# Performance work log

Hardware: AMD Instinct MI355X
Metric: run time of the kernel (lower is better)

## Reference

```python
import jax, jax.numpy as jnp
import numpy as np

V, E, H, L, S, B = 32000, 512, 1024, 2, 512, 32


def setup_inputs() -> dict:
    key = jax.random.key(0)
    ks = jax.random.split(key, 12)
    s = 0.05  # keep activations in a sane range
    return {
        "x": jax.random.randint(ks[0], (S, B), 0, V),
        "embed": jax.random.normal(ks[1], (V, E), dtype=jnp.float32) * s,
        "W_ih0": jax.random.normal(ks[2], (4 * H, E), dtype=jnp.float32) * s,
        "W_hh0": jax.random.normal(ks[3], (4 * H, H), dtype=jnp.float32) * s,
        "b_ih0": jax.random.normal(ks[4], (4 * H,), dtype=jnp.float32) * s,
        "b_hh0": jax.random.normal(ks[5], (4 * H,), dtype=jnp.float32) * s,
        "W_ih1": jax.random.normal(ks[6], (4 * H, H), dtype=jnp.float32) * s,
        "W_hh1": jax.random.normal(ks[7], (4 * H, H), dtype=jnp.float32) * s,
        "b_ih1": jax.random.normal(ks[8], (4 * H,), dtype=jnp.float32) * s,
        "b_hh1": jax.random.normal(ks[9], (4 * H,), dtype=jnp.float32) * s,
        "h0": jax.random.normal(ks[10], (L, B, H), dtype=jnp.float32) * s,
        "c0": jax.random.normal(ks[11], (L, B, H), dtype=jnp.float32) * s,
    }


def _lstm_cell(x_t, h_prev, c_prev, Wi, Wh, bi, bh):
    # PyTorch gate order: input, forget, cell(g), output
    gates = x_t @ Wi.T + h_prev @ Wh.T + bi + bh  # [B, 4H]
    i, f, g, o = jnp.split(gates, 4, axis=-1)
    i = jax.nn.sigmoid(i)
    f = jax.nn.sigmoid(f)
    g = jnp.tanh(g)
    o = jax.nn.sigmoid(o)
    c_new = f * c_prev + i * g
    h_new = o * jnp.tanh(c_new)
    return h_new, c_new


def reference(x, embed, W_ih0, W_hh0, b_ih0, b_hh0,
              W_ih1, W_hh1, b_ih1, b_hh1, h0, c0):
    emb = embed[x]  # [S, B, E]; dropout p=0.0 -> identity
    layers = ((W_ih0, W_hh0, b_ih0, b_hh0), (W_ih1, W_hh1, b_ih1, b_hh1))

    def step(carry, e_t):
        h, c = carry  # each [L, B, H]
        inp = e_t
        new_h, new_c = [], []
        for l, (Wi, Wh, bi, bh) in enumerate(layers):
            h_l, c_l = _lstm_cell(inp, h[l], c[l], Wi, Wh, bi, bh)
            new_h.append(h_l)
            new_c.append(c_l)
            inp = h_l  # inter-layer dropout p=0.0 -> identity
        h = jnp.stack(new_h)
        c = jnp.stack(new_c)
        return (h, c), (inp, h, c)

    (_, _), (outs, hiddens, cells) = jax.lax.scan(step, (h0, c0), emb)
    outputs = outs[:, None, :, :]  # match torch shape [S, 1, B, H]
    return outputs, hiddens, cells
```

## Files before the change

### kernel.cpp

```cpp
#include <hip/hip_runtime.h>
#include <hip/hip_cooperative_groups.h>

namespace cg = cooperative_groups;


#define S_LEN 512
#define BATCH 32
#define HID   1024
#define EMB   512
#define NBLK  128
#define NTHR  512

typedef short  bf16x8 __attribute__((ext_vector_type(8)));
typedef float  f32x4  __attribute__((ext_vector_type(4)));

union U8 { bf16x8 v; unsigned short us[8]; uint4 u4; unsigned long long ull[2]; };

__device__ __forceinline__ unsigned short f2bf(float f) {
    unsigned u = __float_as_uint(f);
    u += 0x7fffu + ((u >> 16) & 1u);
    return (unsigned short)(u >> 16);
}

__device__ __forceinline__ uint4 pack8(float4 lo, float4 hi) {
    U8 r;
    r.us[0] = f2bf(lo.x); r.us[1] = f2bf(lo.y); r.us[2] = f2bf(lo.z); r.us[3] = f2bf(lo.w);
    r.us[4] = f2bf(hi.x); r.us[5] = f2bf(hi.y); r.us[6] = f2bf(hi.z); r.us[7] = f2bf(hi.w);
    return r.u4;
}

__device__ __forceinline__ f32x4 mfma16(bf16x8 a, bf16x8 b, f32x4 c) {
    return __builtin_amdgcn_mfma_f32_16x16x32_bf16(a, b, c, 0, 0, 0);
}

__device__ __forceinline__ U8 ld_ws16(const uint4* p) {
    const unsigned long long* q = (const unsigned long long*)p;
    U8 r;
    r.ull[0] = __hip_atomic_load(q,     __ATOMIC_RELAXED, __HIP_MEMORY_SCOPE_AGENT);
    r.ull[1] = __hip_atomic_load(q + 1, __ATOMIC_RELAXED, __HIP_MEMORY_SCOPE_AGENT);
    return r;
}
__device__ __forceinline__ void st_ws16(uint4* p, U8 v) {
    unsigned long long* q = (unsigned long long*)p;
    __hip_atomic_store(q,     v.ull[0], __ATOMIC_RELAXED, __HIP_MEMORY_SCOPE_AGENT);
    __hip_atomic_store(q + 1, v.ull[1], __ATOMIC_RELAXED, __HIP_MEMORY_SCOPE_AGENT);
}

__device__ __forceinline__ float sigm(float x) {
    return __builtin_amdgcn_rcpf(1.0f + __expf(-x));
}
__device__ __forceinline__ float tanh_fast(float x) {
    const float xc = fminf(fmaxf(x, -15.f), 15.f);
    const float t  = __expf(2.f * xc);
    return (t - 1.f) * __builtin_amdgcn_rcpf(t + 1.f);
}

__device__ __forceinline__ void poll64(const int* flags, int target) {
    const int* p = flags + ((threadIdx.x & 63) << 4);
    for (;;) {
        const int v = __hip_atomic_load(p, __ATOMIC_RELAXED, __HIP_MEMORY_SCOPE_AGENT);
        if (__all(v >= target)) break;
        __builtin_amdgcn_s_sleep(1);
    }
}

__global__ __launch_bounds__(NTHR, 1)
void lstm_pipe(const int* __restrict__ x, const float* __restrict__ embed,
               const float* __restrict__ Wi0, const float* __restrict__ Wh0,
               const float* __restrict__ bi0, const float* __restrict__ bh0,
               const float* __restrict__ Wi1, const float* __restrict__ Wh1,
               const float* __restrict__ bi1, const float* __restrict__ bh1,
               const float* __restrict__ h0in, const float* __restrict__ c0in,
               float* __restrict__ outputs, float* __restrict__ hiddens,
               float* __restrict__ cells, uint4* __restrict__ ws)
{
    __shared__ f32x4 sRed[8][8][64];
    __shared__ float sGates[32][68];
    __shared__ unsigned short sHex[32][16];
    __shared__ float sBias[16][4];
    uint4* sEmb = (uint4*)&sRed[0][0][0];

    const int tid  = threadIdx.x;
    const int lane = tid & 63;
    const int wv   = tid >> 6;
    const int bx   = blockIdx.x;
    const bool isL0 = (bx < 64);
    const int g    = isL0 ? bx : bx - 64;

    uint4* h0base = ws;
    uint4* h1base = ws + 16384;
    int*   fbase  = (int*)(ws + 24576);
    int*   flag0  = fbase;
    int*   flag1  = fbase + 1024;

    {
        const int gt = bx * NTHR + tid;
        if (gt < 2048) fbase[gt] = 0;
        if (gt < 8192) {
            const int layer = gt >> 12, kg = (gt >> 5) & 127, b = gt & 31;
            const float* src = h0in + (((size_t)layer << 5) + b) * HID + (kg << 3);
            uint4* dst = layer ? (h1base + 4096) : (h0base + 3 * 4096);
            dst[(kg << 5) + b] = pack8(*(const float4*)src, *(const float4*)(src + 4));
        }
    }
    if (tid < 16) {
        #pragma unroll
        for (int gate = 0; gate < 4; ++gate) {
            const int r = (gate << 10) + (g << 4) + tid;
            sBias[tid][gate] = isL0 ? (bi0[r] + bh0[r]) : (bi1[r] + bh1[r]);
        }
    }
    const int pjj = tid & 15;
    const int pb  = tid >> 4;
    const int jg  = (g << 4) + pjj;
    float creg = isL0 ? c0in[(size_t)pb * HID + jg]
                      : c0in[(size_t)(BATCH + pb) * HID + jg];

    const int n_    = lane & 15;
    const int ko_   = (lane >> 4) << 3;
    const int rb_   = ((n_ >> 2) << 10) + (g << 4) + (n_ & 3);
    bf16x8 w0[4][6];
    bf16x8 w1[4][8];
    if (isL0) {
        #pragma unroll
        for (int nt = 0; nt < 4; ++nt) {
            const int r = rb_ + (nt << 2);
            #pragma unroll
            for (int kf = 0; kf < 6; ++kf) {
                const int k = wv * 192 + kf * 32 + ko_;
                const float* src = (k < EMB) ? Wi0 + (size_t)r * EMB + k
                                             : Wh0 + (size_t)r * HID + (k - EMB);
                U8 t; t.u4 = pack8(*(const float4*)src, *(const float4*)(src + 4));
                w0[nt][kf] = t.v;
            }
        }
    } else {
        #pragma unroll
        for (int nt = 0; nt < 4; ++nt) {
            const int r = rb_ + (nt << 2);
            #pragma unroll
            for (int kf = 0; kf < 8; ++kf) {
                const int k = (wv << 8) + kf * 32 + ko_;
                const float* src = (k < HID) ? Wi1 + (size_t)r * HID + k
                                             : Wh1 + (size_t)r * HID + (k - HID);
                U8 t; t.u4 = pack8(*(const float4*)src, *(const float4*)(src + 4));
                w1[nt][kf] = t.v;
            }
        }
    }

    float4 pe[4][2];
    if (isL0) {
        #pragma unroll
        for (int it = 0; it < 4; ++it) {
            const int b = wv + (it << 3);
            const float* src = embed + (size_t)x[b] * EMB + (lane << 3);
            pe[it][0] = *(const float4*)src;
            pe[it][1] = *(const float4*)(src + 4);
        }
    }

    cg::grid_group grid = cg::this_grid();
    grid.sync();

    const size_t BH = (size_t)BATCH * HID;

    if (isL0) {
        for (int s = 0; s < S_LEN; ++s) {
            #pragma unroll
            for (int it = 0; it < 4; ++it)
                sEmb[lane * 33 + wv + (it << 3)] = pack8(pe[it][0], pe[it][1]);
            __syncthreads();

            if (s + 1 < S_LEN) {
                #pragma unroll
                for (int it = 0; it < 4; ++it) {
                    const int b = wv + (it << 3);
                    const float* src = embed + (size_t)x[((s + 1) << 5) + b] * EMB + (lane << 3);
                    pe[it][0] = *(const float4*)src;
                    pe[it][1] = *(const float4*)(src + 4);
                }
            }
            if (wv >= 2) poll64(flag0, s);

            const uint4* h0p = h0base + (((s + 3) & 3) << 12);

            U8 r0[6], r1[6];
            #pragma unroll
            for (int kf = 0; kf < 6; ++kf) {
                const int kfg = wv * 6 + kf;
                if (kfg >= 16) {
                    const int u = (((kfg - 16) << 2) + (lane >> 4)) * 32 + (lane & 15);
                    r0[kf] = ld_ws16(&h0p[u]);
                    r1[kf] = ld_ws16(&h0p[u + 16]);
                }
            }
            f32x4 acc[2][4] = {{{0,0,0,0},{0,0,0,0},{0,0,0,0},{0,0,0,0}},
                               {{0,0,0,0},{0,0,0,0},{0,0,0,0},{0,0,0,0}}};
            #pragma unroll
            for (int kf = 0; kf < 6; ++kf) {
                const int kfg = wv * 6 + kf;
                bf16x8 a0, a1;
                if (kfg < 16) {
                    const int u = ((kfg << 2) + (lane >> 4)) * 33 + (lane & 15);
                    U8 t0; t0.u4 = sEmb[u];      a0 = t0.v;
                    U8 t1; t1.u4 = sEmb[u + 16]; a1 = t1.v;
                } else {
                    a0 = r0[kf].v;
                    a1 = r1[kf].v;
                }
                #pragma unroll
                for (int nt = 0; nt < 4; ++nt) {
                    acc[0][nt] = mfma16(a0, w0[nt][kf], acc[0][nt]);
                    acc[1][nt] = mfma16(a1, w0[nt][kf], acc[1][nt]);
                }
            }
            __syncthreads();
            #pragma unroll
            for (int mt = 0; mt < 2; ++mt)
                #pragma unroll
                for (int nt = 0; nt < 4; ++nt)
                    sRed[wv][(mt << 2) + nt][lane] = acc[mt][nt];
            __syncthreads();
            {
                const int tile = tid >> 6, l = tid & 63;
                f32x4 sum = sRed[0][tile][l];
                #pragma unroll
                for (int w = 1; w < 8; ++w) sum += sRed[w][tile][l];
                const int mt = tile >> 2, nt = tile & 3;
                const int b0 = (mt << 4) + ((l >> 4) << 2);
                const int col = (nt << 4) + (l & 15);
                sGates[b0 + 0][col] = sum[0];
                sGates[b0 + 1][col] = sum[1];
                sGates[b0 + 2][col] = sum[2];
                sGates[b0 + 3][col] = sum[3];
            }
            __syncthreads();
            float cn_out, hn_out;
            {
                const int cb = ((pjj >> 2) << 4) + (pjj & 3);
                const float ii = sigm     (sGates[pb][cb]      + sBias[pjj][0]);
                const float ff = sigm     (sGates[pb][cb + 4]  + sBias[pjj][1]);
                const float gg = tanh_fast(sGates[pb][cb + 8]  + sBias[pjj][2]);
                const float oo = sigm     (sGates[pb][cb + 12] + sBias[pjj][3]);
                cn_out = ff * creg + ii * gg;
                creg = cn_out;
                hn_out = oo * tanh_fast(cn_out);
                sHex[pb][pjj] = f2bf(hn_out);
            }
            __syncthreads();
            if (wv == 0) {
                if (s >= 4) poll64(flag1, s - 3);
                const int b = lane & 31, kgl = lane >> 5;
                U8 hb;
                #pragma unroll
                for (int jj = 0; jj < 8; ++jj) hb.us[jj] = sHex[b][(kgl << 3) + jj];
                st_ws16(h0base + ((s & 3) << 12) + (((g << 1) + kgl) << 5) + b, hb);
                asm volatile("s_waitcnt vmcnt(0)" ::: "memory");
                if (lane == 0)
                    __hip_atomic_store(flag0 + (g << 4), s + 1,
                                       __ATOMIC_RELAXED, __HIP_MEMORY_SCOPE_AGENT);
            }
            cells  [(size_t)(s << 1) * BH + (size_t)pb * HID + jg] = cn_out;
            hiddens[(size_t)(s << 1) * BH + (size_t)pb * HID + jg] = hn_out;
        }
    } else {
        for (int s = 0; s < S_LEN; ++s) {
            if (wv < 4) poll64(flag0, s + 1);
            else        poll64(flag1, s);

            const uint4* h0c = h0base + ((s & 3) << 12);
            const uint4* h1p = h1base + (((s + 1) & 1) << 12);

            U8 r0[8], r1[8];
            #pragma unroll
            for (int kf = 0; kf < 8; ++kf) {
                const int kfg = (wv << 3) + kf;
                const uint4* src = (kfg < 32) ? h0c : h1p;
                const int u = (((kfg & 31) << 2) + (lane >> 4)) * 32 + (lane & 15);
                r0[kf] = ld_ws16(&src[u]);
                r1[kf] = ld_ws16(&src[u + 16]);
            }
            f32x4 acc[2][4] = {{{0,0,0,0},{0,0,0,0},{0,0,0,0},{0,0,0,0}},
                               {{0,0,0,0},{0,0,0,0},{0,0,0,0},{0,0,0,0}}};
            #pragma unroll
            for (int kf = 0; kf < 8; ++kf) {
                #pragma unroll
                for (int nt = 0; nt < 4; ++nt) {
                    acc[0][nt] = mfma16(r0[kf].v, w1[nt][kf], acc[0][nt]);
                    acc[1][nt] = mfma16(r1[kf].v, w1[nt][kf], acc[1][nt]);
                }
            }
            #pragma unroll
            for (int mt = 0; mt < 2; ++mt)
                #pragma unroll
                for (int nt = 0; nt < 4; ++nt)
                    sRed[wv][(mt << 2) + nt][lane] = acc[mt][nt];
            __syncthreads();
            {
                const int tile = tid >> 6, l = tid & 63;
                f32x4 sum = sRed[0][tile][l];
                #pragma unroll
                for (int w = 1; w < 8; ++w) sum += sRed[w][tile][l];
                const int mt = tile >> 2, nt = tile & 3;
                const int b0 = (mt << 4) + ((l >> 4) << 2);
                const int col = (nt << 4) + (l & 15);
                sGates[b0 + 0][col] = sum[0];
                sGates[b0 + 1][col] = sum[1];
                sGates[b0 + 2][col] = sum[2];
                sGates[b0 + 3][col] = sum[3];
            }
            __syncthreads();
            float cn_out, hn_out;
            {
                const int cb = ((pjj >> 2) << 4) + (pjj & 3);
                const float ii = sigm     (sGates[pb][cb]      + sBias[pjj][0]);
                const float ff = sigm     (sGates[pb][cb + 4]  + sBias[pjj][1]);
                const float gg = tanh_fast(sGates[pb][cb + 8]  + sBias[pjj][2]);
                const float oo = sigm     (sGates[pb][cb + 12] + sBias[pjj][3]);
                cn_out = ff * creg + ii * gg;
                creg = cn_out;
                hn_out = oo * tanh_fast(cn_out);
                sHex[pb][pjj] = f2bf(hn_out);
            }
            __syncthreads();
            if (wv == 0) {
                const int b = lane & 31, kgl = lane >> 5;
                U8 hb;
                #pragma unroll
                for (int jj = 0; jj < 8; ++jj) hb.us[jj] = sHex[b][(kgl << 3) + jj];
                st_ws16(h1base + ((s & 1) << 12) + (((g << 1) + kgl) << 5) + b, hb);
                asm volatile("s_waitcnt vmcnt(0)" ::: "memory");
                if (lane == 0)
                    __hip_atomic_store(flag1 + (g << 4), s + 1,
                                       __ATOMIC_RELAXED, __HIP_MEMORY_SCOPE_AGENT);
            }
            {
                const size_t o = (size_t)pb * HID + jg;
                cells  [(size_t)((s << 1) + 1) * BH + o] = cn_out;
                hiddens[(size_t)((s << 1) + 1) * BH + o] = hn_out;
                outputs[(size_t)s * BH + o]              = hn_out;
            }
        }
    }
}

#define KC 256
__global__ __launch_bounds__(256)
void lstm_step(const float* __restrict__ Wi, const float* __restrict__ Wh,
               const float* __restrict__ bi, const float* __restrict__ bh,
               const float* __restrict__ xsrc, const int* __restrict__ xidx, int K1,
               const float* __restrict__ Hprev, const float* __restrict__ Cprev,
               float* __restrict__ Hout, float* __restrict__ Cout,
               float* __restrict__ Hout2)
{
    __shared__ float As[32][KC + 4];
    __shared__ float red[256][5];

    const int t  = threadIdx.x;
    const int b  = t & 31;
    const int jl = (t >> 5) & 1;
    const int ks = t >> 6;
    const int j  = (blockIdx.x << 1) + jl;

    const int Ktot = K1 + HID;
    const int NC   = Ktot / KC;

    float acc0 = 0.f, acc1 = 0.f, acc2 = 0.f, acc3 = 0.f;

    for (int c = 0; c < NC; ++c) {
        const int  k0  = c * KC;
        const bool isX = (k0 < K1);

        #pragma unroll
        for (int i = 0; i < 8; ++i) {
            const int idx4 = t + (i << 8);
            const int row  = idx4 >> 6;
            const int c4   = idx4 & 63;
            const float* src;
            if (isX) {
                const size_t r0 = xidx ? (size_t)xidx[row] : (size_t)row;
                src = xsrc + r0 * (size_t)K1 + k0;
            } else {
                src = Hprev + (size_t)row * HID + (k0 - K1);
            }
            *(float4*)&As[row][c4 << 2] = *(const float4*)(src + (c4 << 2));
        }
        __syncthreads();

        const float* W      = isX ? Wi : Wh;
        const int    stride = isX ? K1 : HID;
        const int    kw     = k0 + (ks << 6) - (isX ? 0 : K1);
        const float* w0 = W + (size_t)(j       ) * stride + kw;
        const float* w1 = W + (size_t)(j + 1024) * stride + kw;
        const float* w2 = W + (size_t)(j + 2048) * stride + kw;
        const float* w3 = W + (size_t)(j + 3072) * stride + kw;
        const float* a  = &As[b][ks << 6];

        #pragma unroll 4
        for (int kk = 0; kk < 64; kk += 4) {
            const float4 av = *(const float4*)(a + kk);
            float4 w;
            w = *(const float4*)(w0 + kk);
            acc0 = fmaf(av.x, w.x, acc0); acc0 = fmaf(av.y, w.y, acc0);
            acc0 = fmaf(av.z, w.z, acc0); acc0 = fmaf(av.w, w.w, acc0);
            w = *(const float4*)(w1 + kk);
            acc1 = fmaf(av.x, w.x, acc1); acc1 = fmaf(av.y, w.y, acc1);
            acc1 = fmaf(av.z, w.z, acc1); acc1 = fmaf(av.w, w.w, acc1);
            w = *(const float4*)(w2 + kk);
            acc2 = fmaf(av.x, w.x, acc2); acc2 = fmaf(av.y, w.y, acc2);
            acc2 = fmaf(av.z, w.z, acc2); acc2 = fmaf(av.w, w.w, acc2);
            w = *(const float4*)(w3 + kk);
            acc3 = fmaf(av.x, w.x, acc3); acc3 = fmaf(av.y, w.y, acc3);
            acc3 = fmaf(av.z, w.z, acc3); acc3 = fmaf(av.w, w.w, acc3);
        }
        __syncthreads();
    }

    red[t][0] = acc0; red[t][1] = acc1; red[t][2] = acc2; red[t][3] = acc3;
    __syncthreads();

    if (t < 64) {
        float tot[4];
        #pragma unroll
        for (int gg = 0; gg < 4; ++gg) {
            const int r = j + (gg << 10);
            tot[gg] = red[t][gg] + red[t + 64][gg] + red[t + 128][gg] + red[t + 192][gg]
                   + bi[r] + bh[r];
        }
        const float ig = 1.f / (1.f + expf(-tot[0]));
        const float fg = 1.f / (1.f + expf(-tot[1]));
        const float gv = tanhf(tot[2]);
        const float og = 1.f / (1.f + expf(-tot[3]));
        const size_t o  = (size_t)b * HID + j;
        const float  cp = Cprev[o];
        const float  cn = fg * cp + ig * gv;
        const float  hn = og * tanhf(cn);
        Cout[o] = cn;
        Hout[o] = hn;
        if (Hout2) Hout2[o] = hn;
    }
}

extern "C" void kernel_launch(void* const* d_in, const int* in_sizes, int n_in,
                              void* d_out, int out_size, void* d_ws, size_t ws_size,
                              hipStream_t stream)
{
    (void)in_sizes; (void)n_in; (void)out_size;

    const int*   x     = (const int*)  d_in[0];
    const float* embed = (const float*)d_in[1];
    const float* Wi0   = (const float*)d_in[2];
    const float* Wh0   = (const float*)d_in[3];
    const float* bi0   = (const float*)d_in[4];
    const float* bh0   = (const float*)d_in[5];
    const float* Wi1   = (const float*)d_in[6];
    const float* Wh1   = (const float*)d_in[7];
    const float* bi1   = (const float*)d_in[8];
    const float* bh1   = (const float*)d_in[9];
    const float* h0in  = (const float*)d_in[10];
    const float* c0in  = (const float*)d_in[11];

    float* out     = (float*)d_out;
    const size_t BH = (size_t)BATCH * HID;
    float* outputs = out;
    float* hiddens = out + (size_t)S_LEN * BH;
    float* cells   = out + 3 * (size_t)S_LEN * BH;
    uint4* ws      = (uint4*)d_ws;

    bool coop_ok = (ws_size >= 401408);
    if (coop_ok) {
        void* args[] = {
            (void*)&x, (void*)&embed,
            (void*)&Wi0, (void*)&Wh0, (void*)&bi0, (void*)&bh0,
            (void*)&Wi1, (void*)&Wh1, (void*)&bi1, (void*)&bh1,
            (void*)&h0in, (void*)&c0in,
            (void*)&outputs, (void*)&hiddens, (void*)&cells, (void*)&ws
        };
        hipError_t e = hipLaunchCooperativeKernel((void*)lstm_pipe,
                                                  dim3(NBLK), dim3(NTHR), args, 0, stream);
        if (e != hipSuccess) { (void)hipGetLastError(); coop_ok = false; }
    }
    if (!coop_ok) {
        for (int s = 0; s < S_LEN; ++s) {
            const float* Hp0 = s ? hiddens + ((size_t)(s - 1) * 2 + 0) * BH : h0in;
            const float* Cp0 = s ? cells   + ((size_t)(s - 1) * 2 + 0) * BH : c0in;
            float* H0o = hiddens + ((size_t)s * 2 + 0) * BH;
            float* C0o = cells   + ((size_t)s * 2 + 0) * BH;
            lstm_step<<<512, 256, 0, stream>>>(Wi0, Wh0, bi0, bh0,
                                               embed, x + (size_t)s * BATCH, EMB,
                                               Hp0, Cp0, H0o, C0o, nullptr);

            const float* Hp1 = s ? hiddens + ((size_t)(s - 1) * 2 + 1) * BH : h0in + BH;
            const float* Cp1 = s ? cells   + ((size_t)(s - 1) * 2 + 1) * BH : c0in + BH;
            float* H1o = hiddens + ((size_t)s * 2 + 1) * BH;
            float* C1o = cells   + ((size_t)s * 2 + 1) * BH;
            lstm_step<<<512, 256, 0, stream>>>(Wi1, Wh1, bi1, bh1,
                                               H0o, nullptr, HID,
                                               Hp1, Cp1, H1o, C1o, outputs + (size_t)s * BH);
        }
    }
}
```

Measured before the change: 3.453 ms.

## Defer h publication to next step and narrow flag polling per wave

Restructures the persistent LSTM pipeline step loop. The h broadcast and flag store move to wave 7 at the start of the next iteration, and that wave's output stores are deferred too, which removes a __syncthreads per step. The embedding tile is double-buffered in its own LDS array and prefetched two steps ahead. Each wave now polls only the producer flags for the h slice it reads instead of all 64. This shortens the per-step critical path, at the cost of more LDS use and more complex ordering between the deferred flag store and consumers.

```diff
diff --git a/kernel.cpp b/kernel.cpp
--- a/kernel.cpp
+++ b/kernel.cpp
@@ -57,6 +57,16 @@
 
 __device__ __forceinline__ void poll64(const int* flags, int target) {
     const int* p = flags + ((threadIdx.x & 63) << 4);
+    for (;;) {
+        const int v = __hip_atomic_load(p, __ATOMIC_RELAXED, __HIP_MEMORY_SCOPE_AGENT);
+        if (__all(v >= target)) break;
+        __builtin_amdgcn_s_sleep(1);
+    }
+}
+__device__ __forceinline__ void pollsub(const int* flags, int base, int cnt, int target) {
+    const int l   = threadIdx.x & 63;
+    const int idx = (l < cnt) ? l : 0;
+    const int* p  = flags + ((base + idx) << 4);
     for (;;) {
         const int v = __hip_atomic_load(p, __ATOMIC_RELAXED, __HIP_MEMORY_SCOPE_AGENT);
         if (__all(v >= target)) break;
@@ -75,10 +85,10 @@
                float* __restrict__ cells, uint4* __restrict__ ws)
 {
     __shared__ f32x4 sRed[8][8][64];
+    __shared__ uint4 sEmbBuf[2][64 * 33];
     __shared__ float sGates[32][68];
     __shared__ unsigned short sHex[32][16];
     __shared__ float sBias[16][4];
-    uint4* sEmb = (uint4*)&sRed[0][0][0];
 
     const int tid  = threadIdx.x;
     const int lane = tid & 63;
@@ -116,9 +126,9 @@
     float creg = isL0 ? c0in[(size_t)pb * HID + jg]
                       : c0in[(size_t)(BATCH + pb) * HID + jg];
 
-    const int n_    = lane & 15;
-    const int ko_   = (lane >> 4) << 3;
-    const int rb_   = ((n_ >> 2) << 10) + (g << 4) + (n_ & 3);
+    const int n_  = lane & 15;
+    const int ko_ = (lane >> 4) << 3;
+    const int rb_ = ((n_ >> 2) << 10) + (g << 4) + (n_ & 3);
     bf16x8 w0[4][6];
     bf16x8 w1[4][8];
     if (isL0) {
@@ -155,6 +165,12 @@
         for (int it = 0; it < 4; ++it) {
             const int b = wv + (it << 3);
             const float* src = embed + (size_t)x[b] * EMB + (lane << 3);
+            sEmbBuf[0][lane * 33 + b] = pack8(*(const float4*)src, *(const float4*)(src + 4));
+        }
+        #pragma unroll
+        for (int it = 0; it < 4; ++it) {
+            const int b = wv + (it << 3);
+            const float* src = embed + (size_t)x[32 + b] * EMB + (lane << 3);
             pe[it][0] = *(const float4*)src;
             pe[it][1] = *(const float4*)(src + 4);
         }
@@ -164,37 +180,68 @@
     grid.sync();
 
     const size_t BH = (size_t)BATCH * HID;
+    float pendC = 0.f, pendH = 0.f;
 
     if (isL0) {
         for (int s = 0; s < S_LEN; ++s) {
-            #pragma unroll
-            for (int it = 0; it < 4; ++it)
-                sEmb[lane * 33 + wv + (it << 3)] = pack8(pe[it][0], pe[it][1]);
             __syncthreads();
 
-            if (s + 1 < S_LEN) {
+            U8 r0[6], r1[6];
+            if (wv == 7) {
+                if (s > 0) {
+                    const int b = lane & 31, kgl = lane >> 5;
+                    U8 hb;
+                    #pragma unroll
+                    for (int jj = 0; jj < 8; ++jj) hb.us[jj] = sHex[b][(kgl << 3) + jj];
+                    st_ws16(h0base + (((s - 1) & 3) << 12) + (((g << 1) + kgl) << 5) + b, hb);
+                }
+                if (s + 1 < S_LEN) {
+                    #pragma unroll
+                    for (int it = 0; it < 4; ++it)
+                        sEmbBuf[(s + 1) & 1][lane * 33 + wv + (it << 3)] = pack8(pe[it][0], pe[it][1]);
+                }
+                if (s > 0) {
+                    asm volatile("s_waitcnt vmcnt(0)" ::: "memory");
+                    if (lane == 0)
+                        __hip_atomic_store(flag0 + (g << 4), s,
+                                           __ATOMIC_RELAXED, __HIP_MEMORY_SCOPE_AGENT);
+                    cells  [(size_t)((s - 1) << 1) * BH + (size_t)pb * HID + jg] = pendC;
+                    hiddens[(size_t)((s - 1) << 1) * BH + (size_t)pb * HID + jg] = pendH;
+                }
+                if (s >= 4) poll64(flag1, s - 3);
+            } else if (s + 1 < S_LEN) {
+                #pragma unroll
+                for (int it = 0; it < 4; ++it)
+                    sEmbBuf[(s + 1) & 1][lane * 33 + wv + (it << 3)] = pack8(pe[it][0], pe[it][1]);
+            }
+
+            if (wv >= 2) {
+                const int fst = (wv * 6 < 16) ? 16 : wv * 6;
+                const int pb0 = (fst - 16) << 1;
+                const int pct = ((wv * 6 + 6 - 16) << 1) - pb0;
+                pollsub(flag0, pb0, pct, s);
+                const uint4* h0p = h0base + (((s + 3) & 3) << 12);
+                #pragma unroll
+                for (int kf = 0; kf < 6; ++kf) {
+                    const int kfg = wv * 6 + kf;
+                    if (kfg >= 16) {
+                        const int u = (((kfg - 16) << 2) + (lane >> 4)) * 32 + (lane & 15);
+                        r0[kf] = ld_ws16(&h0p[u]);
+                        r1[kf] = ld_ws16(&h0p[u + 16]);
+                    }
+                }
+            }
+            if (s + 2 < S_LEN) {
                 #pragma unroll
                 for (int it = 0; it < 4; ++it) {
                     const int b = wv + (it << 3);
-                    const float* src = embed + (size_t)x[((s + 1) << 5) + b] * EMB + (lane << 3);
+                    const float* src = embed + (size_t)x[((s + 2) << 5) + b] * EMB + (lane << 3);
                     pe[it][0] = *(const float4*)src;
                     pe[it][1] = *(const float4*)(src + 4);
                 }
             }
-            if (wv >= 2) poll64(flag0, s);
-
-            const uint4* h0p = h0base + (((s + 3) & 3) << 12);
-
-            U8 r0[6], r1[6];
-            #pragma unroll
-            for (int kf = 0; kf < 6; ++kf) {
-                const int kfg = wv * 6 + kf;
-                if (kfg >= 16) {
-                    const int u = (((kfg - 16) << 2) + (lane >> 4)) * 32 + (lane & 15);
-                    r0[kf] = ld_ws16(&h0p[u]);
-                    r1[kf] = ld_ws16(&h0p[u + 16]);
-                }
-            }
+
+            const uint4* eb = sEmbBuf[s & 1];
             f32x4 acc[2][4] = {{{0,0,0,0},{0,0,0,0},{0,0,0,0},{0,0,0,0}},
                                {{0,0,0,0},{0,0,0,0},{0,0,0,0},{0,0,0,0}}};
             #pragma unroll
@@ -203,8 +250,8 @@
                 bf16x8 a0, a1;
                 if (kfg < 16) {
                     const int u = ((kfg << 2) + (lane >> 4)) * 33 + (lane & 15);
-                    U8 t0; t0.u4 = sEmb[u];      a0 = t0.v;
-                    U8 t1; t1.u4 = sEmb[u + 16]; a1 = t1.v;
+                    U8 t0; t0.u4 = eb[u];      a0 = t0.v;
+                    U8 t1; t1.u4 = eb[u + 16]; a1 = t1.v;
                 } else {
                     a0 = r0[kf].v;
                     a1 = r1[kf].v;
@@ -215,7 +262,6 @@
                     acc[1][nt] = mfma16(a1, w0[nt][kf], acc[1][nt]);
                 }
             }
-            __syncthreads();
             #pragma unroll
             for (int mt = 0; mt < 2; ++mt)
                 #pragma unroll
@@ -236,42 +282,62 @@
                 sGates[b0 + 3][col] = sum[3];
             }
             __syncthreads();
-            float cn_out, hn_out;
             {
                 const int cb = ((pjj >> 2) << 4) + (pjj & 3);
                 const float ii = sigm     (sGates[pb][cb]      + sBias[pjj][0]);
                 const float ff = sigm     (sGates[pb][cb + 4]  + sBias[pjj][1]);
                 const float gg = tanh_fast(sGates[pb][cb + 8]  + sBias[pjj][2]);
                 const float oo = sigm     (sGates[pb][cb + 12] + sBias[pjj][3]);
-                cn_out = ff * creg + ii * gg;
-                creg = cn_out;
-                hn_out = oo * tanh_fast(cn_out);
-                sHex[pb][pjj] = f2bf(hn_out);
-            }
+                const float cn = ff * creg + ii * gg;
+                creg = cn;
+                const float hn = oo * tanh_fast(cn);
+                sHex[pb][pjj] = f2bf(hn);
+                if (wv < 7) {
+                    cells  [(size_t)(s << 1) * BH + (size_t)pb * HID + jg] = cn;
+                    hiddens[(size_t)(s << 1) * BH + (size_t)pb * HID + jg] = hn;
+                } else { pendC = cn; pendH = hn; }
+            }
+        }
+        __syncthreads();
+        if (wv == 7) {
+            const int b = lane & 31, kgl = lane >> 5;
+            U8 hb;
+            #pragma unroll
+            for (int jj = 0; jj < 8; ++jj) hb.us[jj] = sHex[b][(kgl << 3) + jj];
+            st_ws16(h0base + ((511 & 3) << 12) + (((g << 1) + kgl) << 5) + b, hb);
+            asm volatile("s_waitcnt vmcnt(0)" ::: "memory");
+            if (lane == 0)
+                __hip_atomic_store(flag0 + (g << 4), 512,
+                                   __ATOMIC_RELAXED, __HIP_MEMORY_SCOPE_AGENT);
+            cells  [(size_t)(511 << 1) * BH + (size_t)pb * HID + jg] = pendC;
+            hiddens[(size_t)(511 << 1) * BH + (size_t)pb * HID + jg] = pendH;
+        }
+    } else {
+        float pendO = 0.f;
+        for (int s = 0; s < S_LEN; ++s) {
             __syncthreads();
-            if (wv == 0) {
-                if (s >= 4) poll64(flag1, s - 3);
+
+            if (wv == 7 && s > 0) {
                 const int b = lane & 31, kgl = lane >> 5;
                 U8 hb;
                 #pragma unroll
                 for (int jj = 0; jj < 8; ++jj) hb.us[jj] = sHex[b][(kgl << 3) + jj];
-                st_ws16(h0base + ((s & 3) << 12) + (((g << 1) + kgl) << 5) + b, hb);
+                st_ws16(h1base + (((s - 1) & 1) << 12) + (((g << 1) + kgl) << 5) + b, hb);
                 asm volatile("s_waitcnt vmcnt(0)" ::: "memory");
                 if (lane == 0)
-                    __hip_atomic_store(flag0 + (g << 4), s + 1,
+                    __hip_atomic_store(flag1 + (g << 4), s,
                                        __ATOMIC_RELAXED, __HIP_MEMORY_SCOPE_AGENT);
-            }
-            cells  [(size_t)(s << 1) * BH + (size_t)pb * HID + jg] = cn_out;
-            hiddens[(size_t)(s << 1) * BH + (size_t)pb * HID + jg] = hn_out;
-        }
-    } else {
-        for (int s = 0; s < S_LEN; ++s) {
-            if (wv < 4) poll64(flag0, s + 1);
-            else        poll64(flag1, s);
+                const size_t o = (size_t)pb * HID + jg;
+                cells  [(size_t)(((s - 1) << 1) + 1) * BH + o] = pendC;
+                hiddens[(size_t)(((s - 1) << 1) + 1) * BH + o] = pendH;
+                outputs[(size_t)(s - 1) * BH + o]              = pendO;
+            }
+
+            if (wv < 4) pollsub(flag0, wv << 4, 16, s + 1);
+            else        pollsub(flag1, (wv - 4) << 4, 16, s);
 
             const uint4* h0c = h0base + ((s & 3) << 12);
             const uint4* h1p = h1base + (((s + 1) & 1) << 12);
-
             U8 r0[8], r1[8];
             #pragma unroll
             for (int kf = 0; kf < 8; ++kf) {
@@ -311,36 +377,30 @@
                 sGates[b0 + 3][col] = sum[3];
             }
             __syncthreads();
-            float cn_out, hn_out;
             {
                 const int cb = ((pjj >> 2) << 4) + (pjj & 3);
                 const float ii = sigm     (sGates[pb][cb]      + sBias[pjj][0]);
                 const float ff = sigm     (sGates[pb][cb + 4]  + sBias[pjj][1]);
                 const float gg = tanh_fast(sGates[pb][cb + 8]  + sBias[pjj][2]);
                 const float oo = sigm     (sGates[pb][cb + 12] + sBias[pjj][3]);
-                cn_out = ff * creg + ii * gg;
-                creg = cn_out;
-                hn_out = oo * tanh_fast(cn_out);
-                sHex[pb][pjj] = f2bf(hn_out);
-            }
-            __syncthreads();
-            if (wv == 0) {
-                const int b = lane & 31, kgl = lane >> 5;
-                U8 hb;
-                #pragma unroll
-                for (int jj = 0; jj < 8; ++jj) hb.us[jj] = sHex[b][(kgl << 3) + jj];
-                st_ws16(h1base + ((s & 1) << 12) + (((g << 1) + kgl) << 5) + b, hb);
-                asm volatile("s_waitcnt vmcnt(0)" ::: "memory");
-                if (lane == 0)
-                    __hip_atomic_store(flag1 + (g << 4), s + 1,
-                                       __ATOMIC_RELAXED, __HIP_MEMORY_SCOPE_AGENT);
-            }
-            {
-                const size_t o = (size_t)pb * HID + jg;
-                cells  [(size_t)((s << 1) + 1) * BH + o] = cn_out;
-                hiddens[(size_t)((s << 1) + 1) * BH + o] = hn_out;
-                outputs[(size_t)s * BH + o]              = hn_out;
-            }
+                const float cn = ff * creg + ii * gg;
+                creg = cn;
+                const float hn = oo * tanh_fast(cn);
+                sHex[pb][pjj] = f2bf(hn);
+                if (wv < 7) {
+                    const size_t o = (size_t)pb * HID + jg;
+                    cells  [(size_t)((s << 1) + 1) * BH + o] = cn;
+                    hiddens[(size_t)((s << 1) + 1) * BH + o] = hn;
+                    outputs[(size_t)s * BH + o]              = hn;
+                } else { pendC = cn; pendH = hn; pendO = hn; }
+            }
+        }
+        __syncthreads();
+        if (wv == 7) {
+            const size_t o = (size_t)pb * HID + jg;
+            cells  [(size_t)((511 << 1) + 1) * BH + o] = pendC;
+            hiddens[(size_t)((511 << 1) + 1) * BH + o] = pendH;
+            outputs[(size_t)511 * BH + o]              = pendO;
         }
     }
 }
```

Result: slower. 3.942 ms (+14.2%).

## Shorten per-step critical path in pipelined LSTM with deeper ring and wave-0 cell update

Applied to the files above, without the earlier changes.

Layer-0 h ring buffer grows from 4 to 8 slots so layer 0 can run further ahead of layer 1. The elementwise cell update now runs entirely in wave 0, with 8 columns per lane and vectorized output stores, which removes one block-wide barrier and the sHex staging. Embedding staging moves into its own shared buffer and is prefetched two steps ahead outside the critical region. In layer 1, wave 0 prefetches the next step's layer-0 h right after publishing. In exchange, the workspace requirement grows, which could make the cooperative path fall back if the buffer is too small. The gate math is also serialized onto a single wave.

```diff
diff --git a/kernel.cpp b/kernel.cpp
--- a/kernel.cpp
+++ b/kernel.cpp
@@ -10,6 +10,7 @@
 #define EMB   512
 #define NBLK  128
 #define NTHR  512
+#define RING0 8
 
 typedef short  bf16x8 __attribute__((ext_vector_type(8)));
 typedef float  f32x4  __attribute__((ext_vector_type(4)));
@@ -75,10 +76,9 @@
                float* __restrict__ cells, uint4* __restrict__ ws)
 {
     __shared__ f32x4 sRed[8][8][64];
-    __shared__ float sGates[32][68];
-    __shared__ unsigned short sHex[32][16];
+    __shared__ uint4 sEmb[64 * 33];
+    __shared__ float sGates[32][69];
     __shared__ float sBias[16][4];
-    uint4* sEmb = (uint4*)&sRed[0][0][0];
 
     const int tid  = threadIdx.x;
     const int lane = tid & 63;
@@ -88,8 +88,8 @@
     const int g    = isL0 ? bx : bx - 64;
 
     uint4* h0base = ws;
-    uint4* h1base = ws + 16384;
-    int*   fbase  = (int*)(ws + 24576);
+    uint4* h1base = ws + 32768;
+    int*   fbase  = (int*)(ws + 40960);
     int*   flag0  = fbase;
     int*   flag1  = fbase + 1024;
 
@@ -99,7 +99,7 @@
         if (gt < 8192) {
             const int layer = gt >> 12, kg = (gt >> 5) & 127, b = gt & 31;
             const float* src = h0in + (((size_t)layer << 5) + b) * HID + (kg << 3);
-            uint4* dst = layer ? (h1base + 4096) : (h0base + 3 * 4096);
+            uint4* dst = layer ? (h1base + 4096) : (h0base + (RING0 - 1) * 4096);
             dst[(kg << 5) + b] = pack8(*(const float4*)src, *(const float4*)(src + 4));
         }
     }
@@ -110,15 +110,20 @@
             sBias[tid][gate] = isL0 ? (bi0[r] + bh0[r]) : (bi1[r] + bh1[r]);
         }
     }
-    const int pjj = tid & 15;
-    const int pb  = tid >> 4;
-    const int jg  = (g << 4) + pjj;
-    float creg = isL0 ? c0in[(size_t)pb * HID + jg]
-                      : c0in[(size_t)(BATCH + pb) * HID + jg];
-
-    const int n_    = lane & 15;
-    const int ko_   = (lane >> 4) << 3;
-    const int rb_   = ((n_ >> 2) << 10) + (g << 4) + (n_ & 3);
+
+    const int b0_   = lane & 31;
+    const int half_ = lane >> 5;
+    float creg[8];
+    if (wv == 0) {
+        #pragma unroll
+        for (int c = 0; c < 8; ++c)
+            creg[c] = c0in[(size_t)((isL0 ? 0 : BATCH) + b0_) * HID
+                           + (g << 4) + (half_ << 3) + c];
+    }
+
+    const int n_  = lane & 15;
+    const int ko_ = (lane >> 4) << 3;
+    const int rb_ = ((n_ >> 2) << 10) + (g << 4) + (n_ & 3);
     bf16x8 w0[4][6];
     bf16x8 w1[4][8];
     if (isL0) {
@@ -155,6 +160,12 @@
         for (int it = 0; it < 4; ++it) {
             const int b = wv + (it << 3);
             const float* src = embed + (size_t)x[b] * EMB + (lane << 3);
+            sEmb[lane * 33 + b] = pack8(*(const float4*)src, *(const float4*)(src + 4));
+        }
+        #pragma unroll
+        for (int it = 0; it < 4; ++it) {
+            const int b = wv + (it << 3);
+            const float* src = embed + (size_t)x[32 + b] * EMB + (lane << 3);
             pe[it][0] = *(const float4*)src;
             pe[it][1] = *(const float4*)(src + 4);
         }
@@ -167,32 +178,18 @@
 
     if (isL0) {
         for (int s = 0; s < S_LEN; ++s) {
-            #pragma unroll
-            for (int it = 0; it < 4; ++it)
-                sEmb[lane * 33 + wv + (it << 3)] = pack8(pe[it][0], pe[it][1]);
-            __syncthreads();
-
-            if (s + 1 < S_LEN) {
-                #pragma unroll
-                for (int it = 0; it < 4; ++it) {
-                    const int b = wv + (it << 3);
-                    const float* src = embed + (size_t)x[((s + 1) << 5) + b] * EMB + (lane << 3);
-                    pe[it][0] = *(const float4*)src;
-                    pe[it][1] = *(const float4*)(src + 4);
-                }
-            }
-            if (wv >= 2) poll64(flag0, s);
-
-            const uint4* h0p = h0base + (((s + 3) & 3) << 12);
-
             U8 r0[6], r1[6];
-            #pragma unroll
-            for (int kf = 0; kf < 6; ++kf) {
-                const int kfg = wv * 6 + kf;
-                if (kfg >= 16) {
-                    const int u = (((kfg - 16) << 2) + (lane >> 4)) * 32 + (lane & 15);
-                    r0[kf] = ld_ws16(&h0p[u]);
-                    r1[kf] = ld_ws16(&h0p[u + 16]);
+            if (wv >= 2) {
+                poll64(flag0, s);
+                const uint4* h0p = h0base + (((s + RING0 - 1) & (RING0 - 1)) << 12);
+                #pragma unroll
+                for (int kf = 0; kf < 6; ++kf) {
+                    const int kfg = wv * 6 + kf;
+                    if (kfg >= 16) {
+                        const int u = (((kfg - 16) << 2) + (lane >> 4)) * 32 + (lane & 15);
+                        r0[kf] = ld_ws16(&h0p[u]);
+                        r1[kf] = ld_ws16(&h0p[u + 16]);
+                    }
                 }
             }
             f32x4 acc[2][4] = {{{0,0,0,0},{0,0,0,0},{0,0,0,0},{0,0,0,0}},
@@ -215,13 +212,27 @@
                     acc[1][nt] = mfma16(a1, w0[nt][kf], acc[1][nt]);
                 }
             }
-            __syncthreads();
             #pragma unroll
             for (int mt = 0; mt < 2; ++mt)
                 #pragma unroll
                 for (int nt = 0; nt < 4; ++nt)
                     sRed[wv][(mt << 2) + nt][lane] = acc[mt][nt];
             __syncthreads();
+
+            if (s + 1 < S_LEN) {
+                #pragma unroll
+                for (int it = 0; it < 4; ++it)
+                    sEmb[lane * 33 + wv + (it << 3)] = pack8(pe[it][0], pe[it][1]);
+            }
+            if (s + 2 < S_LEN) {
+                #pragma unroll
+                for (int it = 0; it < 4; ++it) {
+                    const int b = wv + (it << 3);
+                    const float* src = embed + (size_t)x[((s + 2) << 5) + b] * EMB + (lane << 3);
+                    pe[it][0] = *(const float4*)src;
+                    pe[it][1] = *(const float4*)(src + 4);
+                }
+            }
             {
                 const int tile = tid >> 6, l = tid & 63;
                 f32x4 sum = sRed[0][tile][l];
@@ -236,59 +247,86 @@
                 sGates[b0 + 3][col] = sum[3];
             }
             __syncthreads();
-            float cn_out, hn_out;
-            {
-                const int cb = ((pjj >> 2) << 4) + (pjj & 3);
-                const float ii = sigm     (sGates[pb][cb]      + sBias[pjj][0]);
-                const float ff = sigm     (sGates[pb][cb + 4]  + sBias[pjj][1]);
-                const float gg = tanh_fast(sGates[pb][cb + 8]  + sBias[pjj][2]);
-                const float oo = sigm     (sGates[pb][cb + 12] + sBias[pjj][3]);
-                cn_out = ff * creg + ii * gg;
-                creg = cn_out;
-                hn_out = oo * tanh_fast(cn_out);
-                sHex[pb][pjj] = f2bf(hn_out);
-            }
-            __syncthreads();
+
             if (wv == 0) {
-                if (s >= 4) poll64(flag1, s - 3);
-                const int b = lane & 31, kgl = lane >> 5;
+                if (s >= RING0) poll64(flag1, s - (RING0 - 1));
                 U8 hb;
-                #pragma unroll
-                for (int jj = 0; jj < 8; ++jj) hb.us[jj] = sHex[b][(kgl << 3) + jj];
-                st_ws16(h0base + ((s & 3) << 12) + (((g << 1) + kgl) << 5) + b, hb);
+                float hv[8], cv[8];
+                #pragma unroll
+                for (int c = 0; c < 8; ++c) {
+                    const int pjj = (half_ << 3) + c;
+                    const int cb  = ((pjj >> 2) << 4) + (pjj & 3);
+                    const float ii = sigm     (sGates[b0_][cb]      + sBias[pjj][0]);
+                    const float ff = sigm     (sGates[b0_][cb + 4]  + sBias[pjj][1]);
+                    const float gg = tanh_fast(sGates[b0_][cb + 8]  + sBias[pjj][2]);
+                    const float oo = sigm     (sGates[b0_][cb + 12] + sBias[pjj][3]);
+                    const float cn = ff * creg[c] + ii * gg;
+                    creg[c] = cn;
+                    const float hn = oo * tanh_fast(cn);
+                    cv[c] = cn; hv[c] = hn;
+                    hb.us[c] = f2bf(hn);
+                }
+                st_ws16(h0base + ((s & (RING0 - 1)) << 12)
+                        + (((g << 1) + half_) << 5) + b0_, hb);
                 asm volatile("s_waitcnt vmcnt(0)" ::: "memory");
                 if (lane == 0)
                     __hip_atomic_store(flag0 + (g << 4), s + 1,
                                        __ATOMIC_RELAXED, __HIP_MEMORY_SCOPE_AGENT);
-            }
-            cells  [(size_t)(s << 1) * BH + (size_t)pb * HID + jg] = cn_out;
-            hiddens[(size_t)(s << 1) * BH + (size_t)pb * HID + jg] = hn_out;
+                float* cp = cells   + (size_t)(s << 1) * BH + (size_t)b0_ * HID + (g << 4) + (half_ << 3);
+                float* hp = hiddens + (size_t)(s << 1) * BH + (size_t)b0_ * HID + (g << 4) + (half_ << 3);
+                *(float4*)cp       = make_float4(cv[0], cv[1], cv[2], cv[3]);
+                *(float4*)(cp + 4) = make_float4(cv[4], cv[5], cv[6], cv[7]);
+                *(float4*)hp       = make_float4(hv[0], hv[1], hv[2], hv[3]);
+                *(float4*)(hp + 4) = make_float4(hv[4], hv[5], hv[6], hv[7]);
+            }
         }
     } else {
-        for (int s = 0; s < S_LEN; ++s) {
-            if (wv < 4) poll64(flag0, s + 1);
-            else        poll64(flag1, s);
-
-            const uint4* h0c = h0base + ((s & 3) << 12);
-            const uint4* h1p = h1base + (((s + 1) & 1) << 12);
-
-            U8 r0[8], r1[8];
+        U8 p0[8], p1[8];
+        if (wv == 0) {
+            poll64(flag0, 1);
+            const uint4* h0c = h0base;
             #pragma unroll
             for (int kf = 0; kf < 8; ++kf) {
-                const int kfg = (wv << 3) + kf;
-                const uint4* src = (kfg < 32) ? h0c : h1p;
-                const int u = (((kfg & 31) << 2) + (lane >> 4)) * 32 + (lane & 15);
-                r0[kf] = ld_ws16(&src[u]);
-                r1[kf] = ld_ws16(&src[u + 16]);
+                const int u = ((kf << 2) + (lane >> 4)) * 32 + (lane & 15);
+                p0[kf] = ld_ws16(&h0c[u]);
+                p1[kf] = ld_ws16(&h0c[u + 16]);
+            }
+        }
+        for (int s = 0; s < S_LEN; ++s) {
+            U8 r0[8], r1[8];
+            if (wv > 0) {
+                if (wv < 4) poll64(flag0, s + 1);
+                else        poll64(flag1, s);
+                const uint4* h0c = h0base + ((s & (RING0 - 1)) << 12);
+                const uint4* h1p = h1base + (((s + 1) & 1) << 12);
+                #pragma unroll
+                for (int kf = 0; kf < 8; ++kf) {
+                    const int kfg = (wv << 3) + kf;
+                    const uint4* src = (kfg < 32) ? h0c : h1p;
+                    const int u = (((kfg & 31) << 2) + (lane >> 4)) * 32 + (lane & 15);
+                    r0[kf] = ld_ws16(&src[u]);
+                    r1[kf] = ld_ws16(&src[u + 16]);
+                }
             }
             f32x4 acc[2][4] = {{{0,0,0,0},{0,0,0,0},{0,0,0,0},{0,0,0,0}},
                                {{0,0,0,0},{0,0,0,0},{0,0,0,0},{0,0,0,0}}};
-            #pragma unroll
-            for (int kf = 0; kf < 8; ++kf) {
-                #pragma unroll
-                for (int nt = 0; nt < 4; ++nt) {
-                    acc[0][nt] = mfma16(r0[kf].v, w1[nt][kf], acc[0][nt]);
-                    acc[1][nt] = mfma16(r1[kf].v, w1[nt][kf], acc[1][nt]);
+            if (wv == 0) {
+                #pragma unroll
+                for (int kf = 0; kf < 8; ++kf) {
+                    #pragma unroll
+                    for (int nt = 0; nt < 4; ++nt) {
+                        acc[0][nt] = mfma16(p0[kf].v, w1[nt][kf], acc[0][nt]);
+                        acc[1][nt] = mfma16(p1[kf].v, w1[nt][kf], acc[1][nt]);
+                    }
+                }
+            } else {
+                #pragma unroll
+                for (int kf = 0; kf < 8; ++kf) {
+                    #pragma unroll
+                    for (int nt = 0; nt < 4; ++nt) {
+                        acc[0][nt] = mfma16(r0[kf].v, w1[nt][kf], acc[0][nt]);
+                        acc[1][nt] = mfma16(r1[kf].v, w1[nt][kf], acc[1][nt]);
+                    }
                 }
             }
             #pragma unroll
@@ -311,35 +349,50 @@
                 sGates[b0 + 3][col] = sum[3];
             }
             __syncthreads();
-            float cn_out, hn_out;
-            {
-                const int cb = ((pjj >> 2) << 4) + (pjj & 3);
-                const float ii = sigm     (sGates[pb][cb]      + sBias[pjj][0]);
-                const float ff = sigm     (sGates[pb][cb + 4]  + sBias[pjj][1]);
-                const float gg = tanh_fast(sGates[pb][cb + 8]  + sBias[pjj][2]);
-                const float oo = sigm     (sGates[pb][cb + 12] + sBias[pjj][3]);
-                cn_out = ff * creg + ii * gg;
-                creg = cn_out;
-                hn_out = oo * tanh_fast(cn_out);
-                sHex[pb][pjj] = f2bf(hn_out);
-            }
-            __syncthreads();
+
             if (wv == 0) {
-                const int b = lane & 31, kgl = lane >> 5;
                 U8 hb;
-                #pragma unroll
-                for (int jj = 0; jj < 8; ++jj) hb.us[jj] = sHex[b][(kgl << 3) + jj];
-                st_ws16(h1base + ((s & 1) << 12) + (((g << 1) + kgl) << 5) + b, hb);
+                float hv[8], cv[8];
+                #pragma unroll
+                for (int c = 0; c < 8; ++c) {
+                    const int pjj = (half_ << 3) + c;
+                    const int cb  = ((pjj >> 2) << 4) + (pjj & 3);
+                    const float ii = sigm     (sGates[b0_][cb]      + sBias[pjj][0]);
+                    const float ff = sigm     (sGates[b0_][cb + 4]  + sBias[pjj][1]);
+                    const float gg = tanh_fast(sGates[b0_][cb + 8]  + sBias[pjj][2]);
+                    const float oo = sigm     (sGates[b0_][cb + 12] + sBias[pjj][3]);
+                    const float cn = ff * creg[c] + ii * gg;
+                    creg[c] = cn;
+                    const float hn = oo * tanh_fast(cn);
+                    cv[c] = cn; hv[c] = hn;
+                    hb.us[c] = f2bf(hn);
+                }
+                st_ws16(h1base + ((s & 1) << 12)
+                        + (((g << 1) + half_) << 5) + b0_, hb);
                 asm volatile("s_waitcnt vmcnt(0)" ::: "memory");
                 if (lane == 0)
                     __hip_atomic_store(flag1 + (g << 4), s + 1,
                                        __ATOMIC_RELAXED, __HIP_MEMORY_SCOPE_AGENT);
-            }
-            {
-                const size_t o = (size_t)pb * HID + jg;
-                cells  [(size_t)((s << 1) + 1) * BH + o] = cn_out;
-                hiddens[(size_t)((s << 1) + 1) * BH + o] = hn_out;
-                outputs[(size_t)s * BH + o]              = hn_out;
+                if (s + 1 < S_LEN) {
+                    poll64(flag0, s + 2);
+                    const uint4* h0n = h0base + (((s + 1) & (RING0 - 1)) << 12);
+                    #pragma unroll
+                    for (int kf = 0; kf < 8; ++kf) {
+                        const int u = ((kf << 2) + (lane >> 4)) * 32 + (lane & 15);
+                        p0[kf] = ld_ws16(&h0n[u]);
+                        p1[kf] = ld_ws16(&h0n[u + 16]);
+                    }
+                }
+                const size_t ro = (size_t)b0_ * HID + (g << 4) + (half_ << 3);
+                float* cp = cells   + (size_t)((s << 1) + 1) * BH + ro;
+                float* hp = hiddens + (size_t)((s << 1) + 1) * BH + ro;
+                float* op = outputs + (size_t)s * BH + ro;
+                *(float4*)cp       = make_float4(cv[0], cv[1], cv[2], cv[3]);
+                *(float4*)(cp + 4) = make_float4(cv[4], cv[5], cv[6], cv[7]);
+                *(float4*)hp       = make_float4(hv[0], hv[1], hv[2], hv[3]);
+                *(float4*)(hp + 4) = make_float4(hv[4], hv[5], hv[6], hv[7]);
+                *(float4*)op       = make_float4(hv[0], hv[1], hv[2], hv[3]);
+                *(float4*)(op + 4) = make_float4(hv[4], hv[5], hv[6], hv[7]);
             }
         }
     }
@@ -468,7 +521,7 @@
     float* cells   = out + 3 * (size_t)S_LEN * BH;
     uint4* ws      = (uint4*)d_ws;
 
-    bool coop_ok = (ws_size >= 401408);
+    bool coop_ok = (ws_size >= 663552);
     if (coop_ok) {
         void* args[] = {
             (void*)&x, (void*)&embed,
```

After: 4.472 ms. 29.5% more time.

## Embed sequence tags in h exchange words to replace flag-based synchronization

Applied to the files above, without the earlier changes.

Each bf16 hidden value is now stored in a 32-bit word whose upper half holds the step sequence number. Consumers spin on the data itself until every tag matches, which removes the separate flag0 store, the vmcnt(0) wait and the flag poll on the layer-0 to layer-1 path. The exchange buffers drop from four slots to two, so layer 0 now waits on layer-1 progress one step behind instead of three. The cost is twice the workspace traffic per exchange, extra repacking ALU work, and a larger workspace requirement, which moves the cooperative-path threshold.

```diff
diff --git a/kernel.cpp b/kernel.cpp
--- a/kernel.cpp
+++ b/kernel.cpp
@@ -46,6 +46,19 @@
     __hip_atomic_store(q + 1, v.ull[1], __ATOMIC_RELAXED, __HIP_MEMORY_SCOPE_AGENT);
 }
 
+__device__ __forceinline__ unsigned seqm(const uint4 u, unsigned tgt) {
+    return ((u.x >> 16) ^ tgt) | ((u.y >> 16) ^ tgt) |
+           ((u.z >> 16) ^ tgt) | ((u.w >> 16) ^ tgt);
+}
+__device__ __forceinline__ bf16x8 asm2(const uint4 lo, const uint4 hi) {
+    U8 o;
+    o.u4.x = (lo.x & 0xFFFFu) | (lo.y << 16);
+    o.u4.y = (lo.z & 0xFFFFu) | (lo.w << 16);
+    o.u4.z = (hi.x & 0xFFFFu) | (hi.y << 16);
+    o.u4.w = (hi.z & 0xFFFFu) | (hi.w << 16);
+    return o.v;
+}
+
 __device__ __forceinline__ float sigm(float x) {
     return __builtin_amdgcn_rcpf(1.0f + __expf(-x));
 }
@@ -60,6 +73,13 @@
     for (;;) {
         const int v = __hip_atomic_load(p, __ATOMIC_RELAXED, __HIP_MEMORY_SCOPE_AGENT);
         if (__all(v >= target)) break;
+        __builtin_amdgcn_s_sleep(1);
+    }
+}
+__device__ __forceinline__ void probe(const uint4* p, unsigned tgt) {
+    for (;;) {
+        U8 u = ld_ws16(p);
+        if (__all(seqm(u.u4, tgt) == 0u)) break;
         __builtin_amdgcn_s_sleep(1);
     }
 }
@@ -89,18 +109,22 @@
 
     uint4* h0base = ws;
     uint4* h1base = ws + 16384;
-    int*   fbase  = (int*)(ws + 24576);
-    int*   flag0  = fbase;
-    int*   flag1  = fbase + 1024;
+    int*   fbase  = (int*)(ws + 32768);
+    int*   flag1  = fbase;
 
     {
         const int gt = bx * NTHR + tid;
         if (gt < 2048) fbase[gt] = 0;
         if (gt < 8192) {
-            const int layer = gt >> 12, kg = (gt >> 5) & 127, b = gt & 31;
-            const float* src = h0in + (((size_t)layer << 5) + b) * HID + (kg << 3);
-            uint4* dst = layer ? (h1base + 4096) : (h0base + 3 * 4096);
-            dst[(kg << 5) + b] = pack8(*(const float4*)src, *(const float4*)(src + 4));
+            const int layer = gt >> 12, kg8 = (gt >> 5) & 127, b = gt & 31;
+            const float* src = h0in + (((size_t)layer << 5) + b) * HID + (kg8 << 3);
+            uint4 lo, hi;
+            lo.x = f2bf(src[0]); lo.y = f2bf(src[1]); lo.z = f2bf(src[2]); lo.w = f2bf(src[3]);
+            hi.x = f2bf(src[4]); hi.y = f2bf(src[5]); hi.z = f2bf(src[6]); hi.w = f2bf(src[7]);
+            uint4* dst = (layer ? h1base : h0base) + 8192
+                         + (kg8 << 6) + b;
+            dst[0]  = lo;
+            dst[32] = hi;
         }
     }
     if (tid < 16) {
@@ -116,9 +140,9 @@
     float creg = isL0 ? c0in[(size_t)pb * HID + jg]
                       : c0in[(size_t)(BATCH + pb) * HID + jg];
 
-    const int n_    = lane & 15;
-    const int ko_   = (lane >> 4) << 3;
-    const int rb_   = ((n_ >> 2) << 10) + (g << 4) + (n_ & 3);
+    const int n_  = lane & 15;
+    const int ko_ = (lane >> 4) << 3;
+    const int rb_ = ((n_ >> 2) << 10) + (g << 4) + (n_ & 3);
     bf16x8 w0[4][6];
     bf16x8 w1[4][8];
     if (isL0) {
@@ -181,18 +205,30 @@
                     pe[it][1] = *(const float4*)(src + 4);
                 }
             }
-            if (wv >= 2) poll64(flag0, s);
-
-            const uint4* h0p = h0base + (((s + 3) & 3) << 12);
-
-            U8 r0[6], r1[6];
-            #pragma unroll
-            for (int kf = 0; kf < 6; ++kf) {
-                const int kfg = wv * 6 + kf;
-                if (kfg >= 16) {
-                    const int u = (((kfg - 16) << 2) + (lane >> 4)) * 32 + (lane & 15);
-                    r0[kf] = ld_ws16(&h0p[u]);
-                    r1[kf] = ld_ws16(&h0p[u + 16]);
+
+            U8 a0lo[6], a0hi[6], a1lo[6], a1hi[6];
+            if (wv >= 2) {
+                const unsigned tgt = (unsigned)s;
+                const uint4* slot = h0base + (((s + 1) & 1) << 13);
+                const int kfg0 = (wv * 6 < 16) ? 16 : wv * 6;
+                probe(slot + ((((kfg0 - 16) << 2) + (lane >> 4)) << 6) + (lane & 15), tgt);
+                for (;;) {
+                    unsigned m = 0;
+                    #pragma unroll
+                    for (int kf = 0; kf < 6; ++kf) {
+                        const int kfg = wv * 6 + kf;
+                        if (kfg >= 16) {
+                            const int kg8 = ((kfg - 16) << 2) + (lane >> 4);
+                            const uint4* u0 = slot + (kg8 << 6) + (lane & 15);
+                            a0lo[kf] = ld_ws16(u0);
+                            a0hi[kf] = ld_ws16(u0 + 32);
+                            a1lo[kf] = ld_ws16(u0 + 16);
+                            a1hi[kf] = ld_ws16(u0 + 48);
+                            m |= seqm(a0lo[kf].u4, tgt) | seqm(a0hi[kf].u4, tgt)
+                               | seqm(a1lo[kf].u4, tgt) | seqm(a1hi[kf].u4, tgt);
+                        }
+                    }
+                    if (__all(m == 0u)) break;
                 }
             }
             f32x4 acc[2][4] = {{{0,0,0,0},{0,0,0,0},{0,0,0,0},{0,0,0,0}},
@@ -206,8 +242,8 @@
                     U8 t0; t0.u4 = sEmb[u];      a0 = t0.v;
                     U8 t1; t1.u4 = sEmb[u + 16]; a1 = t1.v;
                 } else {
-                    a0 = r0[kf].v;
-                    a1 = r1[kf].v;
+                    a0 = asm2(a0lo[kf].u4, a0hi[kf].u4);
+                    a1 = asm2(a1lo[kf].u4, a1hi[kf].u4);
                 }
                 #pragma unroll
                 for (int nt = 0; nt < 4; ++nt) {
@@ -250,45 +286,62 @@
             }
             __syncthreads();
             if (wv == 0) {
-                if (s >= 4) poll64(flag1, s - 3);
+                if (s >= 2) poll64(flag1, s - 1);
                 const int b = lane & 31, kgl = lane >> 5;
-                U8 hb;
-                #pragma unroll
-                for (int jj = 0; jj < 8; ++jj) hb.us[jj] = sHex[b][(kgl << 3) + jj];
-                st_ws16(h0base + ((s & 3) << 12) + (((g << 1) + kgl) << 5) + b, hb);
-                asm volatile("s_waitcnt vmcnt(0)" ::: "memory");
-                if (lane == 0)
-                    __hip_atomic_store(flag0 + (g << 4), s + 1,
-                                       __ATOMIC_RELAXED, __HIP_MEMORY_SCOPE_AGENT);
+                const unsigned sq = (unsigned)(s + 1) << 16;
+                U8 lo, hi;
+                lo.u4.x = sHex[b][(kgl << 3) + 0] | sq;
+                lo.u4.y = sHex[b][(kgl << 3) + 1] | sq;
+                lo.u4.z = sHex[b][(kgl << 3) + 2] | sq;
+                lo.u4.w = sHex[b][(kgl << 3) + 3] | sq;
+                hi.u4.x = sHex[b][(kgl << 3) + 4] | sq;
+                hi.u4.y = sHex[b][(kgl << 3) + 5] | sq;
+                hi.u4.z = sHex[b][(kgl << 3) + 6] | sq;
+                hi.u4.w = sHex[b][(kgl << 3) + 7] | sq;
+                uint4* dst = h0base + ((s & 1) << 13)
+                           + (((g << 2) + (kgl << 1)) << 5) + b;
+                st_ws16(dst,      lo);
+                st_ws16(dst + 32, hi);
             }
             cells  [(size_t)(s << 1) * BH + (size_t)pb * HID + jg] = cn_out;
             hiddens[(size_t)(s << 1) * BH + (size_t)pb * HID + jg] = hn_out;
         }
     } else {
         for (int s = 0; s < S_LEN; ++s) {
-            if (wv < 4) poll64(flag0, s + 1);
-            else        poll64(flag1, s);
-
-            const uint4* h0c = h0base + ((s & 3) << 12);
-            const uint4* h1p = h1base + (((s + 1) & 1) << 12);
-
-            U8 r0[8], r1[8];
-            #pragma unroll
-            for (int kf = 0; kf < 8; ++kf) {
-                const int kfg = (wv << 3) + kf;
-                const uint4* src = (kfg < 32) ? h0c : h1p;
-                const int u = (((kfg & 31) << 2) + (lane >> 4)) * 32 + (lane & 15);
-                r0[kf] = ld_ws16(&src[u]);
-                r1[kf] = ld_ws16(&src[u + 16]);
+            const unsigned tgt = (wv < 4) ? (unsigned)(s + 1) : (unsigned)s;
+            const uint4* slot = (wv < 4) ? h0base + ((s & 1) << 13)
+                                         : h1base + (((s + 1) & 1) << 13);
+            {
+                const int kg8p = (((wv << 3) & 31) << 2) + (lane >> 4);
+                probe(slot + (kg8p << 6) + (lane & 15), tgt);
+            }
+            U8 a0lo[8], a0hi[8], a1lo[8], a1hi[8];
+            for (;;) {
+                unsigned m = 0;
+                #pragma unroll
+                for (int kf = 0; kf < 8; ++kf) {
+                    const int kfg = (wv << 3) + kf;
+                    const int kg8 = ((kfg & 31) << 2) + (lane >> 4);
+                    const uint4* u0 = slot + (kg8 << 6) + (lane & 15);
+                    a0lo[kf] = ld_ws16(u0);
+                    a0hi[kf] = ld_ws16(u0 + 32);
+                    a1lo[kf] = ld_ws16(u0 + 16);
+                    a1hi[kf] = ld_ws16(u0 + 48);
+                    m |= seqm(a0lo[kf].u4, tgt) | seqm(a0hi[kf].u4, tgt)
+                       | seqm(a1lo[kf].u4, tgt) | seqm(a1hi[kf].u4, tgt);
+                }
+                if (__all(m == 0u)) break;
             }
             f32x4 acc[2][4] = {{{0,0,0,0},{0,0,0,0},{0,0,0,0},{0,0,0,0}},
                                {{0,0,0,0},{0,0,0,0},{0,0,0,0},{0,0,0,0}}};
             #pragma unroll
             for (int kf = 0; kf < 8; ++kf) {
+                const bf16x8 a0 = asm2(a0lo[kf].u4, a0hi[kf].u4);
+                const bf16x8 a1 = asm2(a1lo[kf].u4, a1hi[kf].u4);
                 #pragma unroll
                 for (int nt = 0; nt < 4; ++nt) {
-                    acc[0][nt] = mfma16(r0[kf].v, w1[nt][kf], acc[0][nt]);
-                    acc[1][nt] = mfma16(r1[kf].v, w1[nt][kf], acc[1][nt]);
+                    acc[0][nt] = mfma16(a0, w1[nt][kf], acc[0][nt]);
+                    acc[1][nt] = mfma16(a1, w1[nt][kf], acc[1][nt]);
                 }
             }
             #pragma unroll
@@ -326,11 +379,20 @@
             __syncthreads();
             if (wv == 0) {
                 const int b = lane & 31, kgl = lane >> 5;
-                U8 hb;
-                #pragma unroll
-                for (int jj = 0; jj < 8; ++jj) hb.us[jj] = sHex[b][(kgl << 3) + jj];
-                st_ws16(h1base + ((s & 1) << 12) + (((g << 1) + kgl) << 5) + b, hb);
-                asm volatile("s_waitcnt vmcnt(0)" ::: "memory");
+                const unsigned sq = (unsigned)(s + 1) << 16;
+                U8 lo, hi;
+                lo.u4.x = sHex[b][(kgl << 3) + 0] | sq;
+                lo.u4.y = sHex[b][(kgl << 3) + 1] | sq;
+                lo.u4.z = sHex[b][(kgl << 3) + 2] | sq;
+                lo.u4.w = sHex[b][(kgl << 3) + 3] | sq;
+                hi.u4.x = sHex[b][(kgl << 3) + 4] | sq;
+                hi.u4.y = sHex[b][(kgl << 3) + 5] | sq;
+                hi.u4.z = sHex[b][(kgl << 3) + 6] | sq;
+                hi.u4.w = sHex[b][(kgl << 3) + 7] | sq;
+                uint4* dst = h1base + ((s & 1) << 13)
+                           + (((g << 2) + (kgl << 1)) << 5) + b;
+                st_ws16(dst,      lo);
+                st_ws16(dst + 32, hi);
                 if (lane == 0)
                     __hip_atomic_store(flag1 + (g << 4), s + 1,
                                        __ATOMIC_RELAXED, __HIP_MEMORY_SCOPE_AGENT);
@@ -468,7 +530,7 @@
     float* cells   = out + 3 * (size_t)S_LEN * BH;
     uint4* ws      = (uint4*)d_ws;
 
-    bool coop_ok = (ws_size >= 401408);
+    bool coop_ok = (ws_size >= 532480);
     if (coop_ok) {
         void* args[] = {
             (void*)&x, (void*)&embed,
```

After: 8.067 ms. +133.6%, slower.
